# Optimization experiments

Hardware: AMD Instinct MI355X
Metric: run time of the kernel (lower is better)

Reference implementation:

```python
import jax, jax.numpy as jnp
import numpy as np

MAX_HOPS = 3


def setup_inputs() -> dict:
    key = jax.random.key(0)
    ks = jax.random.split(key, 6)
    B, M, S = 128, 200, 20
    V, D = 100000, 128
    NC, CL = 10000, 10
    stories = jax.random.randint(ks[0], (B, M, S), 0, V, dtype=jnp.int64)
    queries = jax.random.randint(ks[1], (B, S), 0, V, dtype=jnp.int64)
    candidates = jax.random.randint(ks[2], (NC, CL), 0, V, dtype=jnp.int64)
    # 0.05 scale keeps hop softmax logits in a sane range
    A_tab = jax.random.normal(ks[3], (V, D), dtype=jnp.float32) * 0.05
    W_tab = jax.random.normal(ks[4], (V, D), dtype=jnp.float32) * 0.05
    H_w = jax.random.normal(ks[5], (D, D), dtype=jnp.float32) * 0.05
    return {"stories": stories, "queries": queries, "candidates": candidates,
            "A_tab": A_tab, "W_tab": W_tab, "H_w": H_w}


def reference(stories, queries, candidates, A_tab, W_tab, H_w):
    # padding_idx=0: embedding row 0 is zero
    A = A_tab.at[0].set(0.0)
    W = W_tab.at[0].set(0.0)
    # query encoding: gather + sum-pool -> [B, D]
    u = jnp.sum(A[queries], axis=1)
    # memory encoding: [B, M, D] (same A table each hop, as in the source)
    m = jnp.sum(A[stories], axis=2)
    for _ in range(MAX_HOPS):
        dotted = jnp.einsum('bmd,bd->bm', m, u)          # attention logits
        probs = jax.nn.softmax(dotted, axis=1)           # [B, M]
        o = jnp.einsum('bm,bmd->bd', probs, m)           # weighted memory sum
        u = jnp.tanh(u @ H_w.T + o)                      # Linear(no bias) + tanh
    cand_sum = jnp.sum(W[candidates], axis=1)            # [NC, D]
    logits = u @ cand_sum.T                              # [B, NC]
    return logits
```

## Files before the change

kernel.cpp:

```cpp
#include <hip/hip_runtime.h>
#include <hip/hip_bf16.h>
#include <math.h>

#define BB 128
#define MM 200
#define SS 20
#define DD 128
#define NC 10000
#define CL 10
#define LCT 64
#define NROW (BB * MM)
#define NV 100000

#define CND_OFF 0
#define CND_BLK (NC / 8)
#define CONV_OFF CND_BLK
#define CONV_BLK (NV / 16)
#define QRY_OFF (CONV_OFF + CONV_BLK)
#define QRY_BLK (BB / 16)
#define PREP_BLK (QRY_OFF + QRY_BLK)
#define SG_BLK (NROW / 32)

__device__ __forceinline__ unsigned pack_bf16(float a, float b) {
    unsigned ua = __float_as_uint(a), ub = __float_as_uint(b);
    ua += 0x7fff + ((ua >> 16) & 1);
    ub += 0x7fff + ((ub >> 16) & 1);
    return (ua >> 16) | (ub & 0xffff0000u);
}
__device__ __forceinline__ float bflo(unsigned v) { return __uint_as_float(v << 16); }
__device__ __forceinline__ float bfhi(unsigned v) { return __uint_as_float(v & 0xffff0000u); }

__device__ __forceinline__ int detect_shift(const int* __restrict__ q) {
    int zc = 0;
#pragma unroll
    for (int i = 0; i < 8; ++i) zc += (q[2 * i + 1] == 0);
    return (zc >= 6) ? 1 : 0;
}

__device__ __forceinline__ void acc_i8(unsigned w, float s, float* a) {
    a[0] = fmaf(s, (float)(int)(signed char)(w & 0xffu), a[0]);
    a[1] = fmaf(s, (float)(int)(signed char)((w >> 8) & 0xffu), a[1]);
    a[2] = fmaf(s, (float)(int)(signed char)((w >> 16) & 0xffu), a[2]);
    a[3] = fmaf(s, (float)(int)(signed char)(w >> 24), a[3]);
}

__global__ __launch_bounds__(256) void k_prep(const float* __restrict__ A,
                                              const float* __restrict__ W,
                                              const int* __restrict__ queries,
                                              const int* __restrict__ cands,
                                              unsigned char* __restrict__ Ai8,
                                              float* __restrict__ sc,
                                              float* __restrict__ u0_all,
                                              float* __restrict__ cand_buf) {
    int bid = blockIdx.x;
    int tid = threadIdx.x;

    if (bid < CONV_OFF) {
        int shift = detect_shift(queries);
        int g = tid >> 5, l = tid & 31;
        int row = (bid - CND_OFF) * 8 + g;
        int toks[CL];
#pragma unroll
        for (int s = 0; s < CL; ++s)
            toks[s] = cands[((size_t)(row * CL + s)) << shift];
        float4 acc = make_float4(0.f, 0.f, 0.f, 0.f);
#pragma unroll
        for (int s = 0; s < CL; ++s) {
            float4 v = ((const float4*)(W + (size_t)(unsigned)toks[s] * DD))[l];
            float msk = toks[s] ? 1.f : 0.f;
            acc.x = fmaf(msk, v.x, acc.x);
            acc.y = fmaf(msk, v.y, acc.y);
            acc.z = fmaf(msk, v.z, acc.z);
            acc.w = fmaf(msk, v.w, acc.w);
        }
        ((float4*)(cand_buf + (size_t)row * DD))[l] = acc;
    } else if (bid < QRY_OFF) {
        int g = tid >> 4, l = tid & 15;
        int row = (bid - CONV_OFF) * 16 + g;
        const float4* rp = (const float4*)(A + (size_t)row * DD) + l * 2;
        float4 x0 = rp[0], x1 = rp[1];
        float am = fmaxf(fmaxf(fmaxf(fabsf(x0.x), fabsf(x0.y)),
                               fmaxf(fabsf(x0.z), fabsf(x0.w))),
                         fmaxf(fmaxf(fabsf(x1.x), fabsf(x1.y)),
                               fmaxf(fabsf(x1.z), fabsf(x1.w))));
#pragma unroll
        for (int m = 1; m < 16; m <<= 1) am = fmaxf(am, __shfl_xor(am, m, 16));
        float s = am * (1.f / 127.f);
        float inv = (am > 0.f) ? 127.f / am : 0.f;
        int q0 = __float2int_rn(x0.x * inv), q1 = __float2int_rn(x0.y * inv);
        int q2 = __float2int_rn(x0.z * inv), q3 = __float2int_rn(x0.w * inv);
        int q4 = __float2int_rn(x1.x * inv), q5 = __float2int_rn(x1.y * inv);
        int q6 = __float2int_rn(x1.z * inv), q7 = __float2int_rn(x1.w * inv);
        uint2 o;
        o.x = (q0 & 255) | ((q1 & 255) << 8) | ((q2 & 255) << 16) |
              ((unsigned)(q3 & 255) << 24);
        o.y = (q4 & 255) | ((q5 & 255) << 8) | ((q6 & 255) << 16) |
              ((unsigned)(q7 & 255) << 24);
        if (row == 0) {
            o.x = 0u;
            o.y = 0u;
            s = 0.f;
        }
        ((uint2*)Ai8)[(size_t)row * 16 + l] = o;
        if (l == 0) sc[row] = s;
    } else {
        int shift = detect_shift(queries);
        int g = tid >> 4, l = tid & 15;
        int b = (bid - QRY_OFF) * 16 + g;
        float a[8] = {0.f, 0.f, 0.f, 0.f, 0.f, 0.f, 0.f, 0.f};
#pragma unroll
        for (int s = 0; s < SS; ++s) {
            int tok = queries[((size_t)(b * SS + s)) << shift];
            const float4* vp = (const float4*)(A + (size_t)(unsigned)tok * DD) + l * 2;
            float4 v0 = vp[0], v1 = vp[1];
            float msk = tok ? 1.f : 0.f;
            a[0] = fmaf(msk, v0.x, a[0]); a[1] = fmaf(msk, v0.y, a[1]);
            a[2] = fmaf(msk, v0.z, a[2]); a[3] = fmaf(msk, v0.w, a[3]);
            a[4] = fmaf(msk, v1.x, a[4]); a[5] = fmaf(msk, v1.y, a[5]);
            a[6] = fmaf(msk, v1.z, a[6]); a[7] = fmaf(msk, v1.w, a[7]);
        }
        float4* op = (float4*)(u0_all + (size_t)b * DD + l * 8);
        op[0] = make_float4(a[0], a[1], a[2], a[3]);
        op[1] = make_float4(a[4], a[5], a[6], a[7]);
    }
}

__global__ __launch_bounds__(256) void k_sgather(const int* __restrict__ stories,
                                                 const int* __restrict__ queries,
                                                 const unsigned char* __restrict__ Ai8,
                                                 const float* __restrict__ sc,
                                                 unsigned* __restrict__ m_all) {
    int bid = blockIdx.x;
    int tid = threadIdx.x;
    int shift = detect_shift(queries);
    int g = tid >> 3, l = tid & 7;
    int r = bid * 32 + g;

    float a[16];
#pragma unroll
    for (int i = 0; i < 16; ++i) a[i] = 0.f;
#pragma unroll
    for (int s = 0; s < SS; ++s) {
        int tok = stories[((size_t)(r * SS + s)) << shift];
        uint4 v = ((const uint4*)Ai8)[(size_t)(unsigned)tok * 8 + l];
        float st = sc[(unsigned)tok];
        acc_i8(v.x, st, a + 0);
        acc_i8(v.y, st, a + 4);
        acc_i8(v.z, st, a + 8);
        acc_i8(v.w, st, a + 12);
    }
    uint4 o0, o1;
    o0.x = pack_bf16(a[0], a[1]);
    o0.y = pack_bf16(a[2], a[3]);
    o0.z = pack_bf16(a[4], a[5]);
    o0.w = pack_bf16(a[6], a[7]);
    o1.x = pack_bf16(a[8], a[9]);
    o1.y = pack_bf16(a[10], a[11]);
    o1.z = pack_bf16(a[12], a[13]);
    o1.w = pack_bf16(a[14], a[15]);
    uint4* dst = (uint4*)(m_all + (size_t)r * (DD / 2));
    dst[2 * l] = o0;
    dst[2 * l + 1] = o1;
}

__global__ __launch_bounds__(512) void k_hops(const unsigned* __restrict__ m_all,
                                              const float* __restrict__ u0_all,
                                              const float* __restrict__ Hw,
                                              float* __restrict__ uT) {
    __shared__ unsigned m_s[MM][DD / 2];
    __shared__ float u_s[DD];
    __shared__ float p_s[MM];
    __shared__ float o_part[8][DD];
    __shared__ float red_s;

    int b = blockIdx.x;
    int tid = threadIdx.x;

    {
        const uint4* src = (const uint4*)(m_all + (size_t)b * MM * (DD / 2));
        uint4* dst = (uint4*)&m_s[0][0];
        for (int i = tid; i < MM * (DD / 2) / 4; i += 512) dst[i] = src[i];
    }
    if (tid < DD) u_s[tid] = u0_all[(size_t)b * DD + tid];
    __syncthreads();

    for (int hop = 0; hop < 3; ++hop) {
        if (tid < MM) {
            const float2* u2 = (const float2*)u_s;
            float acc = 0.f;
#pragma unroll 8
            for (int li = 0; li < 64; ++li) {
                int j = (tid + li) & 63;
                unsigned pv = m_s[tid][j];
                float2 uv = u2[j];
                acc += bflo(pv) * uv.x + bfhi(pv) * uv.y;
            }
            p_s[tid] = acc;
        }
        __syncthreads();
        if (tid < 64) {
            float v0 = p_s[tid], v1 = p_s[tid + 64], v2 = p_s[tid + 128];
            float v3 = (tid < 8) ? p_s[tid + 192] : -1e30f;
            float mx = fmaxf(fmaxf(v0, v1), fmaxf(v2, v3));
            for (int off = 32; off; off >>= 1) mx = fmaxf(mx, __shfl_down(mx, off));
            mx = __shfl(mx, 0);
            float e0 = __expf(v0 - mx), e1 = __expf(v1 - mx), e2 = __expf(v2 - mx);
            float e3 = (tid < 8) ? __expf(v3 - mx) : 0.f;
            float sm = e0 + e1 + e2 + e3;
            for (int off = 32; off; off >>= 1) sm += __shfl_down(sm, off);
            p_s[tid] = e0;
            p_s[tid + 64] = e1;
            p_s[tid + 128] = e2;
            if (tid < 8) p_s[tid + 192] = e3;
            if (tid == 0) red_s = 1.f / __shfl(sm, 0);
        }
        __syncthreads();
        {
            int c = tid & 63, h = tid >> 6;
            int mm0 = h * 25;
            float ax = 0.f, ay = 0.f;
#pragma unroll 5
            for (int k = 0; k < 25; ++k) {
                unsigned pv = m_s[mm0 + k][c];
                float p = p_s[mm0 + k];
                ax = fmaf(p, bflo(pv), ax);
                ay = fmaf(p, bfhi(pv), ay);
            }
            o_part[h][2 * c] = ax;
            o_part[h][2 * c + 1] = ay;
        }
        __syncthreads();
        float u_new = 0.f;
        if (tid < DD) {
            float o = 0.f;
#pragma unroll
            for (int h = 0; h < 8; ++h) o += o_part[h][tid];
            float acc = o * red_s;
            const float4* hrow = (const float4*)(Hw + tid * DD);
            const float4* u4 = (const float4*)u_s;
#pragma unroll 8
            for (int j = 0; j < DD / 4; ++j) {
                float4 hv = hrow[j];
                float4 uv = u4[j];
                acc += hv.x * uv.x + hv.y * uv.y + hv.z * uv.z + hv.w * uv.w;
            }
            u_new = tanhf(acc);
        }
        __syncthreads();
        if (tid < DD) u_s[tid] = u_new;
        __syncthreads();
    }
    if (tid < DD) uT[tid * BB + b] = u_s[tid];
}

__global__ __launch_bounds__(256) void k_logits(const float* __restrict__ uT,
                                                const float* __restrict__ cs,
                                                float* __restrict__ out) {
    __shared__ float c_s[DD][LCT + 4];
    int c0 = blockIdx.x * LCT;
    int b0 = blockIdx.y * 32;
    int tid = threadIdx.x;
    {
        int c = tid >> 2, l = tid & 3;
        int row = c0 + c;
        if (row >= NC) row = NC - 1;
        const float4* rp = (const float4*)(cs + (size_t)row * DD);
#pragma unroll
        for (int i = 0; i < 8; ++i) {
            int k = (l << 5) + (i << 2);
            float4 v = rp[(l << 3) + i];
            c_s[k][c] = v.x;
            c_s[k + 1][c] = v.y;
            c_s[k + 2][c] = v.z;
            c_s[k + 3][c] = v.w;
        }
    }
    __syncthreads();
    int tx = tid & 31, ty = tid >> 5;
    const float* cb = &c_s[0][ty << 3];
    const float* up = uT + b0 + tx;
    float acc[8];
#pragma unroll
    for (int j = 0; j < 8; ++j) acc[j] = 0.f;
#pragma unroll 4
    for (int k = 0; k < DD; ++k) {
        float u = up[k * BB];
        float4 ca = *(const float4*)(cb + k * (LCT + 4));
        float4 cc = *(const float4*)(cb + k * (LCT + 4) + 4);
        acc[0] = fmaf(u, ca.x, acc[0]);
        acc[1] = fmaf(u, ca.y, acc[1]);
        acc[2] = fmaf(u, ca.z, acc[2]);
        acc[3] = fmaf(u, ca.w, acc[3]);
        acc[4] = fmaf(u, cc.x, acc[4]);
        acc[5] = fmaf(u, cc.y, acc[5]);
        acc[6] = fmaf(u, cc.z, acc[6]);
        acc[7] = fmaf(u, cc.w, acc[7]);
    }
    if (c0 + (ty << 3) < NC) {
        float* orow = out + (size_t)(b0 + tx) * NC + c0 + (ty << 3);
        ((float4*)orow)[0] = make_float4(acc[0], acc[1], acc[2], acc[3]);
        ((float4*)orow)[1] = make_float4(acc[4], acc[5], acc[6], acc[7]);
    }
}

extern "C" void kernel_launch(void* const* d_in, const int* in_sizes, int n_in,
                              void* d_out, int out_size, void* d_ws, size_t ws_size,
                              hipStream_t stream) {
    const int* stories = (const int*)d_in[0];
    const int* queries = (const int*)d_in[1];
    const int* cands   = (const int*)d_in[2];
    const float* A  = (const float*)d_in[3];
    const float* W  = (const float*)d_in[4];
    const float* Hw = (const float*)d_in[5];
    float* out = (float*)d_out;

    unsigned char* Ai8 = (unsigned char*)d_ws;
    float* sc = (float*)(Ai8 + (size_t)NV * DD);
    float* cand_buf = sc + NV;
    float* uT_buf = cand_buf + (size_t)NC * DD;
    float* u0_buf = uT_buf + (size_t)BB * DD;
    unsigned* m_all = (unsigned*)(u0_buf + (size_t)BB * DD);

    k_prep<<<PREP_BLK, 256, 0, stream>>>(A, W, queries, cands, Ai8, sc,
                                         u0_buf, cand_buf);
    k_sgather<<<SG_BLK, 256, 0, stream>>>(stories, queries, Ai8, sc, m_all);
    k_hops<<<BB, 512, 0, stream>>>(m_all, u0_buf, Hw, uT_buf);
    dim3 lgrid((NC + LCT - 1) / LCT, 4);
    k_logits<<<lgrid, 256, 0, stream>>>(uT_buf, cand_buf, out);
}
```

Measured before the change: 182.5 us.

## Drop int8 table quantization and gather stories directly from fp32 A

Removes the pass that quantized the whole 100k-row A table to int8 with per-row scales, and the separate story-gather kernel that read that table. Stories are now summed straight from the fp32 A rows, inside the same launch that gathers the query and candidate rows, which cuts one kernel launch and the full-table read and write. In exchange each story token now fetches a 512-byte fp32 row instead of a 128-byte int8 row, so gather traffic per token is four times larger.

```diff
diff --git a/kernel.cpp b/kernel.cpp
--- a/kernel.cpp
+++ b/kernel.cpp
@@ -12,14 +12,13 @@
 #define NROW (BB * MM)
 #define NV 100000
 
-#define CND_OFF 0
+#define STY_OFF 0
+#define STY_BLK (NROW / 8)
+#define CND_OFF STY_BLK
 #define CND_BLK (NC / 8)
-#define CONV_OFF CND_BLK
-#define CONV_BLK (NV / 16)
-#define QRY_OFF (CONV_OFF + CONV_BLK)
+#define QRY_OFF (CND_OFF + CND_BLK)
 #define QRY_BLK (BB / 16)
-#define PREP_BLK (QRY_OFF + QRY_BLK)
-#define SG_BLK (NROW / 32)
+#define GTH_BLK (QRY_OFF + QRY_BLK)
 
 __device__ __forceinline__ unsigned pack_bf16(float a, float b) {
     unsigned ua = __float_as_uint(a), ub = __float_as_uint(b);
@@ -37,26 +36,37 @@
     return (zc >= 6) ? 1 : 0;
 }
 
-__device__ __forceinline__ void acc_i8(unsigned w, float s, float* a) {
-    a[0] = fmaf(s, (float)(int)(signed char)(w & 0xffu), a[0]);
-    a[1] = fmaf(s, (float)(int)(signed char)((w >> 8) & 0xffu), a[1]);
-    a[2] = fmaf(s, (float)(int)(signed char)((w >> 16) & 0xffu), a[2]);
-    a[3] = fmaf(s, (float)(int)(signed char)(w >> 24), a[3]);
-}
-
-__global__ __launch_bounds__(256) void k_prep(const float* __restrict__ A,
-                                              const float* __restrict__ W,
-                                              const int* __restrict__ queries,
-                                              const int* __restrict__ cands,
-                                              unsigned char* __restrict__ Ai8,
-                                              float* __restrict__ sc,
-                                              float* __restrict__ u0_all,
-                                              float* __restrict__ cand_buf) {
+__global__ __launch_bounds__(256) void k_gather(const int* __restrict__ stories,
+                                                const int* __restrict__ queries,
+                                                const int* __restrict__ cands,
+                                                const float* __restrict__ A,
+                                                const float* __restrict__ W,
+                                                unsigned* __restrict__ m_all,
+                                                float* __restrict__ u0_all,
+                                                float* __restrict__ cand_buf) {
     int bid = blockIdx.x;
     int tid = threadIdx.x;
-
-    if (bid < CONV_OFF) {
-        int shift = detect_shift(queries);
+    int shift = detect_shift(queries);
+
+    if (bid < CND_OFF) {
+        int g = tid >> 5, l = tid & 31;
+        int r = bid * 8 + g;
+        float a0 = 0.f, a1 = 0.f, a2 = 0.f, a3 = 0.f;
+#pragma unroll
+        for (int s = 0; s < SS; ++s) {
+            int tok = stories[((size_t)(r * SS + s)) << shift];
+            float4 v = ((const float4*)(A + (size_t)(unsigned)tok * DD))[l];
+            float msk = tok ? 1.f : 0.f;
+            a0 = fmaf(msk, v.x, a0);
+            a1 = fmaf(msk, v.y, a1);
+            a2 = fmaf(msk, v.z, a2);
+            a3 = fmaf(msk, v.w, a3);
+        }
+        uint2 o;
+        o.x = pack_bf16(a0, a1);
+        o.y = pack_bf16(a2, a3);
+        ((uint2*)(m_all + (size_t)r * (DD / 2)))[l] = o;
+    } else if (bid < QRY_OFF) {
         int g = tid >> 5, l = tid & 31;
         int row = (bid - CND_OFF) * 8 + g;
         int toks[CL];
@@ -74,37 +84,7 @@
             acc.w = fmaf(msk, v.w, acc.w);
         }
         ((float4*)(cand_buf + (size_t)row * DD))[l] = acc;
-    } else if (bid < QRY_OFF) {
-        int g = tid >> 4, l = tid & 15;
-        int row = (bid - CONV_OFF) * 16 + g;
-        const float4* rp = (const float4*)(A + (size_t)row * DD) + l * 2;
-        float4 x0 = rp[0], x1 = rp[1];
-        float am = fmaxf(fmaxf(fmaxf(fabsf(x0.x), fabsf(x0.y)),
-                               fmaxf(fabsf(x0.z), fabsf(x0.w))),
-                         fmaxf(fmaxf(fabsf(x1.x), fabsf(x1.y)),
-                               fmaxf(fabsf(x1.z), fabsf(x1.w))));
-#pragma unroll
-        for (int m = 1; m < 16; m <<= 1) am = fmaxf(am, __shfl_xor(am, m, 16));
-        float s = am * (1.f / 127.f);
-        float inv = (am > 0.f) ? 127.f / am : 0.f;
-        int q0 = __float2int_rn(x0.x * inv), q1 = __float2int_rn(x0.y * inv);
-        int q2 = __float2int_rn(x0.z * inv), q3 = __float2int_rn(x0.w * inv);
-        int q4 = __float2int_rn(x1.x * inv), q5 = __float2int_rn(x1.y * inv);
-        int q6 = __float2int_rn(x1.z * inv), q7 = __float2int_rn(x1.w * inv);
-        uint2 o;
-        o.x = (q0 & 255) | ((q1 & 255) << 8) | ((q2 & 255) << 16) |
-              ((unsigned)(q3 & 255) << 24);
-        o.y = (q4 & 255) | ((q5 & 255) << 8) | ((q6 & 255) << 16) |
-              ((unsigned)(q7 & 255) << 24);
-        if (row == 0) {
-            o.x = 0u;
-            o.y = 0u;
-            s = 0.f;
-        }
-        ((uint2*)Ai8)[(size_t)row * 16 + l] = o;
-        if (l == 0) sc[row] = s;
     } else {
-        int shift = detect_shift(queries);
         int g = tid >> 4, l = tid & 15;
         int b = (bid - QRY_OFF) * 16 + g;
         float a[8] = {0.f, 0.f, 0.f, 0.f, 0.f, 0.f, 0.f, 0.f};
@@ -123,44 +103,6 @@
         op[0] = make_float4(a[0], a[1], a[2], a[3]);
         op[1] = make_float4(a[4], a[5], a[6], a[7]);
     }
-}
-
-__global__ __launch_bounds__(256) void k_sgather(const int* __restrict__ stories,
-                                                 const int* __restrict__ queries,
-                                                 const unsigned char* __restrict__ Ai8,
-                                                 const float* __restrict__ sc,
-                                                 unsigned* __restrict__ m_all) {
-    int bid = blockIdx.x;
-    int tid = threadIdx.x;
-    int shift = detect_shift(queries);
-    int g = tid >> 3, l = tid & 7;
-    int r = bid * 32 + g;
-
-    float a[16];
-#pragma unroll
-    for (int i = 0; i < 16; ++i) a[i] = 0.f;
-#pragma unroll
-    for (int s = 0; s < SS; ++s) {
-        int tok = stories[((size_t)(r * SS + s)) << shift];
-        uint4 v = ((const uint4*)Ai8)[(size_t)(unsigned)tok * 8 + l];
-        float st = sc[(unsigned)tok];
-        acc_i8(v.x, st, a + 0);
-        acc_i8(v.y, st, a + 4);
-        acc_i8(v.z, st, a + 8);
-        acc_i8(v.w, st, a + 12);
-    }
-    uint4 o0, o1;
-    o0.x = pack_bf16(a[0], a[1]);
-    o0.y = pack_bf16(a[2], a[3]);
-    o0.z = pack_bf16(a[4], a[5]);
-    o0.w = pack_bf16(a[6], a[7]);
-    o1.x = pack_bf16(a[8], a[9]);
-    o1.y = pack_bf16(a[10], a[11]);
-    o1.z = pack_bf16(a[12], a[13]);
-    o1.w = pack_bf16(a[14], a[15]);
-    uint4* dst = (uint4*)(m_all + (size_t)r * (DD / 2));
-    dst[2 * l] = o0;
-    dst[2 * l + 1] = o1;
 }
 
 __global__ __launch_bounds__(512) void k_hops(const unsigned* __restrict__ m_all,
@@ -314,16 +256,13 @@
     const float* Hw = (const float*)d_in[5];
     float* out = (float*)d_out;
 
-    unsigned char* Ai8 = (unsigned char*)d_ws;
-    float* sc = (float*)(Ai8 + (size_t)NV * DD);
-    float* cand_buf = sc + NV;
+    float* cand_buf = (float*)d_ws;
     float* uT_buf = cand_buf + (size_t)NC * DD;
     float* u0_buf = uT_buf + (size_t)BB * DD;
     unsigned* m_all = (unsigned*)(u0_buf + (size_t)BB * DD);
 
-    k_prep<<<PREP_BLK, 256, 0, stream>>>(A, W, queries, cands, Ai8, sc,
-                                         u0_buf, cand_buf);
-    k_sgather<<<SG_BLK, 256, 0, stream>>>(stories, queries, Ai8, sc, m_all);
+    k_gather<<<GTH_BLK, 256, 0, stream>>>(stories, queries, cands, A, W,
+                                          m_all, u0_buf, cand_buf);
     k_hops<<<BB, 512, 0, stream>>>(m_all, u0_buf, Hw, uT_buf);
     dim3 lgrid((NC + LCT - 1) / LCT, 4);
     k_logits<<<lgrid, 256, 0, stream>>>(uT_buf, cand_buf, out);
```

Result: slower. 191.0 us (+4.6%).
